# Optimization experiments

Hardware: AMD Instinct MI355X
Metric: run time of the kernel (lower is better)

## Reference

```python
import jax, jax.numpy as jnp
import numpy as np

HEADS = 8


def _attn_1d(xs, w_qkv, w_proj, heads, scale):
    """xs: [N, C, L] -> [N, C, L]. 1x1 conv == channel matmul."""
    n, c, l = xs.shape
    inner = w_proj.shape[1]
    d = inner // heads
    qkv = jnp.einsum('oc,ncl->nol', w_qkv, xs)          # [N, 3*inner, L]
    q, k, v = jnp.split(qkv, 3, axis=1)                  # each [N, inner, L]
    # [N, heads, L, d]
    q = q.reshape(n, heads, d, l).transpose(0, 1, 3, 2)
    k = k.reshape(n, heads, d, l).transpose(0, 1, 3, 2)
    v = v.reshape(n, heads, d, l).transpose(0, 1, 3, 2)
    attn = jax.nn.softmax(jnp.einsum('nhid,nhjd->nhij', q, k) * scale, axis=-1)
    out = jnp.einsum('nhij,nhjd->nhid', attn, v)         # [N, heads, L, d]
    out = out.transpose(0, 1, 3, 2).reshape(n, inner, l) # [N, inner, L]
    return jnp.einsum('co,nol->ncl', w_proj, out)


def _axial(x, w_qkv, w_proj, heads, scale, axis):
    b, c, h, w = x.shape
    if axis == 'h':
        xs = x.transpose(0, 3, 1, 2).reshape(b * w, c, h)
        out = _attn_1d(xs, w_qkv, w_proj, heads, scale)
        return out.reshape(b, w, c, h).transpose(0, 2, 3, 1)
    else:
        xs = x.transpose(0, 2, 1, 3).reshape(b * h, c, w)
        out = _attn_1d(xs, w_qkv, w_proj, heads, scale)
        return out.reshape(b, h, c, w).transpose(0, 2, 1, 3)


def setup_inputs() -> dict:
    key = jax.random.key(0)
    k1, k2, k3 = jax.random.split(key, 3)
    B, C, H, W = 4, 512, 128, 128
    heads = HEADS
    head_dim = C // heads
    inner = head_dim * heads
    x = jax.random.normal(k1, (B, C, H, W), dtype=jnp.float32)
    w_qkv = jax.random.normal(k2, (inner * 3, C), dtype=jnp.float32) * 0.02
    w_proj = jax.random.normal(k3, (C, inner), dtype=jnp.float32) * 0.02
    return {"x": x, "w_qkv": w_qkv, "w_proj": w_proj}


def reference(x, w_qkv, w_proj):
    c = x.shape[1]
    head_dim = c // HEADS
    scale = head_dim ** (-0.5)
    h_out = _axial(x, w_qkv, w_proj, HEADS, scale, 'h')
    w_out = _axial(h_out, w_qkv, w_proj, HEADS, scale, 'w')
    return x + w_out
```

## Files before the change

kernel.cpp:

```cpp
#include <hip/hip_runtime.h>
#include <hip/hip_bf16.h>
#include <stdint.h>

#define B_ 4
#define S_ 128
#define CH 512

typedef __attribute__((ext_vector_type(8))) __bf16 bf16x8;
typedef __attribute__((ext_vector_type(4))) float  f32x4;

__device__ __forceinline__ unsigned short f2b(float f) {
    union { float f; unsigned u; } v; v.f = f;
    unsigned r = v.u + 0x7FFFu + ((v.u >> 16) & 1u);
    return (unsigned short)(r >> 16);
}

#define GLD_LDS16(gp, lp) \
    __builtin_amdgcn_global_load_lds((const __attribute__((address_space(1))) void*)(gp), \
                                     (__attribute__((address_space(3))) void*)(lp), 16, 0, 0)

__global__ void cvt_w(const float* __restrict__ wq, const float* __restrict__ wp,
                      unsigned short* __restrict__ wqb, unsigned short* __restrict__ wpb) {
    int idx = (blockIdx.x * 256 + threadIdx.x) * 4;
    const float* s; unsigned short* d; int off;
    if (idx < 1536 * 512) { s = wq; d = wqb; off = idx; }
    else                  { s = wp; d = wpb; off = idx - 1536 * 512; }
    float4 v = *(const float4*)(s + off);
    ushort4 o; o.x = f2b(v.x); o.y = f2b(v.y); o.z = f2b(v.z); o.w = f2b(v.w);
    *(ushort4*)(d + off) = o;
}

__global__ __launch_bounds__(256) void k0_tr(const float* __restrict__ x,
                                             unsigned short* __restrict__ xb) {
    __shared__ unsigned short t[64][72];
    int bid = blockIdx.x;
    int ct = bid & 7, wt = (bid >> 3) & 1, h = (bid >> 4) & 127, b = bid >> 11;
    int tid = threadIdx.x;
    int c0 = ct * 64, w0 = wt * 64;
    const float* xp = x + ((size_t)b * CH * S_ + h) * S_;
    int wl = (tid & 15) * 4;
#pragma unroll
    for (int it = 0; it < 4; ++it) {
        int c = it * 16 + (tid >> 4);
        float4 v = *(const float4*)(xp + (size_t)(c0 + c) * (S_ * S_) + w0 + wl);
        t[wl + 0][c] = f2b(v.x);
        t[wl + 1][c] = f2b(v.y);
        t[wl + 2][c] = f2b(v.z);
        t[wl + 3][c] = f2b(v.w);
    }
    __syncthreads();
#pragma unroll
    for (int it = 0; it < 2; ++it) {
        int w = it * 32 + (tid >> 3);
        int ce = (tid & 7) * 8;
        int4 v = *(const int4*)&t[w][ce];
        size_t p = (size_t)((b * 128 + w0 + w) * 128 + h);
        *(int4*)(xb + p * 512 + c0 + ce) = v;
    }
}

template<int EPI>
__global__ __launch_bounds__(512, 2) void gemm8(
    const unsigned short* __restrict__ A,
    const unsigned short* __restrict__ Bm,
    unsigned short* __restrict__ outb,
    const float* __restrict__ xres,
    float* __restrict__ outf,
    int Mtiles)
{
    __shared__ unsigned short lds[65536];
    const int NT = 8;
    int nwg = gridDim.x;
    int wg = (blockIdx.x & 7) * (nwg >> 3) + (blockIdx.x >> 3);
    int mb = wg % Mtiles, nb = wg / Mtiles;
    int m0 = mb * 256, n0 = nb * 256;
    int tid = threadIdx.x, lane = tid & 63, wid = tid >> 6;
    int wm = wid >> 2, wn = wid & 3;

    f32x4 acc[8][4] = {};

    int l15  = lane & 15;
    int rsw  = ((lane >> 2) & 3) << 4;
    int cA0  = ((lane >> 4) * 8) ^ rsw;
    int cA1  = (32 + (lane >> 4) * 8) ^ rsw;
    int arow = (wm * 64 + l15) * 64;
    int brow = (wn * 32 + l15) * 64;

    int srow = tid >> 3;
    int scol = ((tid & 7) * 8) ^ (((srow >> 2) & 3) << 4);
    const unsigned short* Ab0 = A  + (size_t)(m0 + srow) * 512 + scol;
    const unsigned short* Bb0 = Bm + (size_t)(n0 + (srow >> 5) * 64 + (srow & 31)) * 512 + scol;

#define STAGE_A(kt, reg) do {                                                  \
        unsigned short* lb_ = &lds[((((kt) & 1) * 2 + (reg)) * 8192)];         \
        const unsigned short* g_ = Ab0 + (size_t)(reg) * (64 * 512) + (kt) * 64;\
        GLD_LDS16(g_,             lb_ + wid * 512);                            \
        GLD_LDS16(g_ + 128 * 512, lb_ + 4096 + wid * 512);                     \
    } while (0)
#define STAGE_B(kt, reg) do {                                                  \
        unsigned short* lb_ = &lds[32768 + ((((kt) & 1) * 2 + (reg)) * 8192)]; \
        const unsigned short* g_ = Bb0 + (size_t)(reg) * (32 * 512) + (kt) * 64;\
        GLD_LDS16(g_,             lb_ + wid * 512);                            \
        GLD_LDS16(g_ + 128 * 512, lb_ + 4096 + wid * 512);                     \
    } while (0)

    STAGE_A(0, 0); STAGE_A(0, 1); STAGE_B(0, 0); STAGE_B(0, 1);
    STAGE_A(1, 0); STAGE_B(1, 0);
    asm volatile("s_waitcnt vmcnt(4)" ::: "memory");
    __builtin_amdgcn_s_barrier();

    for (int j = 0; j < NT; ++j) {
        int db = j & 1;
        bf16x8 af[4][2];
#pragma unroll
        for (int q = 0; q < 4; ++q) {
            const int mq = q >> 1, nq = q & 1;
            int bbase = 32768 + (db * 2 + nq) * 8192 + brow;
            if (nq == 0) {
                int abase = (db * 2 + mq) * 8192 + arow;
#pragma unroll
                for (int fr = 0; fr < 4; ++fr) {
                    af[fr][0] = *(const bf16x8*)&lds[abase + fr * 1024 + cA0];
                    af[fr][1] = *(const bf16x8*)&lds[abase + fr * 1024 + cA1];
                }
            }
            bf16x8 bq[2][2];
#pragma unroll
            for (int fb = 0; fb < 2; ++fb) {
                bq[fb][0] = *(const bf16x8*)&lds[bbase + fb * 1024 + cA0];
                bq[fb][1] = *(const bf16x8*)&lds[bbase + fb * 1024 + cA1];
            }
            if (q == 0)      { if (j + 1 < NT) STAGE_A(j + 1, 1); }
            else if (q == 1) { if (j + 1 < NT) STAGE_B(j + 1, 1); }
            else if (q == 2) { if (j + 2 < NT) STAGE_A(j + 2, 0); }
            else {
                if (j + 2 < NT) STAGE_B(j + 2, 0);
                if (j < NT - 2) asm volatile("s_waitcnt vmcnt(4)" ::: "memory");
                else            asm volatile("s_waitcnt vmcnt(0)" ::: "memory");
            }
            __builtin_amdgcn_s_barrier();
            asm volatile("s_waitcnt lgkmcnt(0)" ::: "memory");
            __builtin_amdgcn_s_setprio(1);
#pragma unroll
            for (int h = 0; h < 2; ++h)
#pragma unroll
                for (int fr = 0; fr < 4; ++fr)
#pragma unroll
                    for (int fb = 0; fb < 2; ++fb)
                        acc[mq * 4 + fr][nq * 2 + fb] = __builtin_amdgcn_mfma_f32_16x16x32_bf16(
                            af[fr][h], bq[fb][h], acc[mq * 4 + fr][nq * 2 + fb], 0, 0, 0);
            __builtin_amdgcn_s_setprio(0);
            __builtin_amdgcn_s_barrier();
        }
    }
#undef STAGE_A
#undef STAGE_B

#pragma unroll
    for (int mi = 0; mi < 8; ++mi) {
        int row0 = m0 + wm * 128 + (mi >> 2) * 64 + (mi & 3) * 16 + ((lane >> 4) << 2);
#pragma unroll
        for (int ni = 0; ni < 4; ++ni) {
            int col = n0 + wn * 64 + (ni >> 1) * 32 + (ni & 1) * 16 + (lane & 15);
            int i = col & 127, sq = (col >> 7) & 127, bb = col >> 14;
            f32x4 a4 = acc[mi][ni];
            if (EPI == 0) {
                int g = row0 >> 6, d0 = row0 & 63;
                if (g < 16) {
                    size_t base = ((size_t)(g * 4 + bb) * 16384 + (size_t)sq * 128 + i) * 64 + d0;
                    ushort4 o;
                    o.x = f2b(a4[0]); o.y = f2b(a4[1]); o.z = f2b(a4[2]); o.w = f2b(a4[3]);
                    *(ushort4*)(outb + base) = o;
                } else {
                    size_t base = ((size_t)(g * 4 + bb) * 8192 + (size_t)sq * 64 + d0) * 128 + i;
                    outb[base]       = f2b(a4[0]);
                    outb[base + 128] = f2b(a4[1]);
                    outb[base + 256] = f2b(a4[2]);
                    outb[base + 384] = f2b(a4[3]);
                }
            } else if (EPI == 1) {
                size_t p2 = ((size_t)bb * 128 + i) * 128 + sq;
                ushort4 o;
                o.x = f2b(a4[0]); o.y = f2b(a4[1]); o.z = f2b(a4[2]); o.w = f2b(a4[3]);
                *(ushort4*)(outb + p2 * 512 + row0) = o;
            } else {
                size_t base = (((size_t)bb * 512 + row0) * 128 + sq) * 128 + i;
#pragma unroll
                for (int r = 0; r < 4; ++r) {
                    size_t a_ = base + (size_t)r * 16384;
                    outf[a_] = xres[a_] + a4[r];
                }
            }
        }
    }
}

__global__ __launch_bounds__(256) void attn_k(const unsigned short* __restrict__ qkv,
                                              unsigned short* __restrict__ o2) {
    __shared__ unsigned short Qs[128 * 80];
    __shared__ unsigned short Ks[128 * 80];
    __shared__ unsigned short Vt[64 * 144];
    int bid = blockIdx.x;
    int t = bid & 7, sq = (bid >> 3) & 127, b = bid >> 10;
    int tid = threadIdx.x, lane = tid & 63, wv = tid >> 6;
    const unsigned short* qg = qkv + ((size_t)(t * 4 + b) * 16384 + (size_t)sq * 128) * 64;
    const unsigned short* kg = qkv + ((size_t)((8 + t) * 4 + b) * 16384 + (size_t)sq * 128) * 64;
    const unsigned short* vg = qkv + ((size_t)((16 + t) * 4 + b) * 8192 + (size_t)sq * 64) * 128;
    {
        int r = tid >> 3, d0 = (tid & 7) * 8;
#pragma unroll
        for (int it = 0; it < 4; ++it) {
            *(int4*)(Qs + (it * 32 + r) * 80 + d0) = *(const int4*)(qg + (it * 32 + r) * 64 + d0);
            *(int4*)(Ks + (it * 32 + r) * 80 + d0) = *(const int4*)(kg + (it * 32 + r) * 64 + d0);
        }
        int r2 = tid >> 4, i0 = (tid & 15) * 8;
#pragma unroll
        for (int it = 0; it < 4; ++it)
            *(int4*)(Vt + (it * 16 + r2) * 144 + i0) = *(const int4*)(vg + (it * 16 + r2) * 128 + i0);
    }
    __syncthreads();

    f32x4 st[8][2] = {};
#pragma unroll
    for (int kk = 0; kk < 2; ++kk) {
        int ko = kk * 32 + (lane >> 4) * 8;
        bf16x8 bq[2];
#pragma unroll
        for (int nt = 0; nt < 2; ++nt)
            bq[nt] = *(const bf16x8*)(Qs + (wv * 32 + nt * 16 + (lane & 15)) * 80 + ko);
#pragma unroll
        for (int mt = 0; mt < 8; ++mt) {
            bf16x8 ak = *(const bf16x8*)(Ks + (mt * 16 + (lane & 15)) * 80 + ko);
#pragma unroll
            for (int nt = 0; nt < 2; ++nt)
                st[mt][nt] = __builtin_amdgcn_mfma_f32_16x16x32_bf16(ak, bq[nt], st[mt][nt], 0, 0, 0);
        }
    }

    const float sc = 0.125f * 1.44269504088896f;
    float mx[2], rinv[2];
    unsigned ppk[8][2][2];
#pragma unroll
    for (int nt = 0; nt < 2; ++nt) {
        float m = -3.0e38f;
#pragma unroll
        for (int mt = 0; mt < 8; ++mt)
#pragma unroll
            for (int r = 0; r < 4; ++r)
                m = fmaxf(m, st[mt][nt][r]);
        m = fmaxf(m, __shfl_xor(m, 16));
        m = fmaxf(m, __shfl_xor(m, 32));
        mx[nt] = m * sc;
    }
#pragma unroll
    for (int nt = 0; nt < 2; ++nt) {
        float s = 0.f;
#pragma unroll
        for (int mt = 0; mt < 8; ++mt) {
            float p0 = exp2f(st[mt][nt][0] * sc - mx[nt]);
            float p1 = exp2f(st[mt][nt][1] * sc - mx[nt]);
            float p2 = exp2f(st[mt][nt][2] * sc - mx[nt]);
            float p3 = exp2f(st[mt][nt][3] * sc - mx[nt]);
            s += (p0 + p1) + (p2 + p3);
            ppk[mt][nt][0] = (unsigned)f2b(p0) | ((unsigned)f2b(p1) << 16);
            ppk[mt][nt][1] = (unsigned)f2b(p2) | ((unsigned)f2b(p3) << 16);
        }
        s += __shfl_xor(s, 16);
        s += __shfl_xor(s, 32);
        rinv[nt] = 1.0f / s;
    }

    f32x4 ov[4][2] = {};
    int g = lane >> 4;
    int ls0 = (lane & 15) | ((g & 1) << 5);
    int ls1 = ls0 | 16;
    int hi = g >> 1;
#pragma unroll
    for (int kt = 0; kt < 4; ++kt) {
        bf16x8 bp[2];
#pragma unroll
        for (int nt = 0; nt < 2; ++nt) {
            unsigned a0 = (unsigned)__shfl((int)ppk[2 * kt    ][nt][0], ls0);
            unsigned b0 = (unsigned)__shfl((int)ppk[2 * kt + 1][nt][0], ls0);
            unsigned a1 = (unsigned)__shfl((int)ppk[2 * kt    ][nt][1], ls0);
            unsigned b1 = (unsigned)__shfl((int)ppk[2 * kt + 1][nt][1], ls0);
            unsigned a2 = (unsigned)__shfl((int)ppk[2 * kt    ][nt][0], ls1);
            unsigned b2 = (unsigned)__shfl((int)ppk[2 * kt + 1][nt][0], ls1);
            unsigned a3 = (unsigned)__shfl((int)ppk[2 * kt    ][nt][1], ls1);
            unsigned b3 = (unsigned)__shfl((int)ppk[2 * kt + 1][nt][1], ls1);
            union { unsigned u[4]; bf16x8 v; } pk;
            pk.u[0] = hi ? b0 : a0;
            pk.u[1] = hi ? b1 : a1;
            pk.u[2] = hi ? b2 : a2;
            pk.u[3] = hi ? b3 : a3;
            bp[nt] = pk.v;
        }
#pragma unroll
        for (int dt = 0; dt < 4; ++dt) {
            bf16x8 av = *(const bf16x8*)(Vt + (dt * 16 + (lane & 15)) * 144 + kt * 32 + (lane >> 4) * 8);
#pragma unroll
            for (int nt = 0; nt < 2; ++nt)
                ov[dt][nt] = __builtin_amdgcn_mfma_f32_16x16x32_bf16(av, bp[nt], ov[dt][nt], 0, 0, 0);
        }
    }

#pragma unroll
    for (int dt = 0; dt < 4; ++dt) {
        int d0 = dt * 16 + (lane >> 4) * 4;
#pragma unroll
        for (int nt = 0; nt < 2; ++nt) {
            int i = wv * 32 + nt * 16 + (lane & 15);
            size_t p = ((size_t)(b * 128 + sq)) * 128 + i;
            ushort4 o;
            o.x = f2b(ov[dt][nt][0] * rinv[nt]);
            o.y = f2b(ov[dt][nt][1] * rinv[nt]);
            o.z = f2b(ov[dt][nt][2] * rinv[nt]);
            o.w = f2b(ov[dt][nt][3] * rinv[nt]);
            *(ushort4*)(o2 + p * 512 + t * 64 + d0) = o;
        }
    }
}

extern "C" void kernel_launch(void* const* d_in, const int* in_sizes, int n_in,
                              void* d_out, int out_size, void* d_ws, size_t ws_size,
                              hipStream_t stream) {
    const float* x  = (const float*)d_in[0];
    const float* wq = (const float*)d_in[1];
    const float* wp = (const float*)d_in[2];
    float* out = (float*)d_out;
    char* ws = (char*)d_ws;
    unsigned short* wqb = (unsigned short*)(ws);
    unsigned short* wpb = (unsigned short*)(ws + ((size_t)2 << 20));
    unsigned short* xb  = (unsigned short*)(ws + ((size_t)4 << 20));
    unsigned short* o2  = (unsigned short*)(ws + ((size_t)68 << 20));
    unsigned short* qkv = (unsigned short*)(ws + ((size_t)132 << 20));

    cvt_w<<<1024, 256, 0, stream>>>(wq, wp, wqb, wpb);
    k0_tr<<<8192, 256, 0, stream>>>(x, xb);
    gemm8<0><<<6 * 256, 512, 0, stream>>>(wqb, xb, qkv, nullptr, nullptr, 6);
    attn_k<<<4096, 256, 0, stream>>>(qkv, o2);
    gemm8<1><<<2 * 256, 512, 0, stream>>>(wpb, o2, xb, nullptr, nullptr, 2);
    gemm8<0><<<6 * 256, 512, 0, stream>>>(wqb, xb, qkv, nullptr, nullptr, 6);
    attn_k<<<4096, 256, 0, stream>>>(qkv, o2);
    gemm8<2><<<2 * 256, 512, 0, stream>>>(wpb, o2, nullptr, x, out, 2);
}
```

Baseline: 584.6 us.

## Reorder GEMM main loop to load all fragments up front and reuse quadrants

Restructures the bf16 GEMM main loop so each k-tile loads the A0/B0 fragments first, then B1/A1, and runs the four MFMA quadrants as (a0,b0),(a0,b1),(a1,b0),(a1,b1). Global-to-LDS staging of the next tiles is spread between the quadrants, and the prefetch depth drops so only A(j+2,0) runs ahead. The aim is to reduce LDS fragment reloads and waits by keeping both A halves in registers, at the cost of higher register pressure and less global prefetch distance. The earlier lgkmcnt waits are removed, so correctness relies on the compiler inserting waits for LDS reads.

Result: slower. 639.2 us (+9.3%).

```diff
diff --git a/kernel.cpp b/kernel.cpp
--- a/kernel.cpp
+++ b/kernel.cpp
@@ -105,54 +105,73 @@
     } while (0)
 
     STAGE_A(0, 0); STAGE_A(0, 1); STAGE_B(0, 0); STAGE_B(0, 1);
-    STAGE_A(1, 0); STAGE_B(1, 0);
-    asm volatile("s_waitcnt vmcnt(4)" ::: "memory");
+    STAGE_A(1, 0);
+    asm volatile("s_waitcnt vmcnt(2)" ::: "memory");
     __builtin_amdgcn_s_barrier();
 
+#define MFMA_Q(ar, br, mo, no)                                                 \
+    __builtin_amdgcn_s_setprio(1);                                             \
+    _Pragma("unroll")                                                          \
+    for (int h = 0; h < 2; ++h)                                                \
+        _Pragma("unroll")                                                      \
+        for (int fr = 0; fr < 4; ++fr)                                         \
+            _Pragma("unroll")                                                  \
+            for (int fb = 0; fb < 2; ++fb)                                     \
+                acc[(mo) + fr][(no) + fb] = __builtin_amdgcn_mfma_f32_16x16x32_bf16( \
+                    ar[fr][h], br[fb][h], acc[(mo) + fr][(no) + fb], 0, 0, 0); \
+    __builtin_amdgcn_s_setprio(0);
+
     for (int j = 0; j < NT; ++j) {
-        int db = j & 1;
-        bf16x8 af[4][2];
-#pragma unroll
-        for (int q = 0; q < 4; ++q) {
-            const int mq = q >> 1, nq = q & 1;
-            int bbase = 32768 + (db * 2 + nq) * 8192 + brow;
-            if (nq == 0) {
-                int abase = (db * 2 + mq) * 8192 + arow;
-#pragma unroll
-                for (int fr = 0; fr < 4; ++fr) {
-                    af[fr][0] = *(const bf16x8*)&lds[abase + fr * 1024 + cA0];
-                    af[fr][1] = *(const bf16x8*)&lds[abase + fr * 1024 + cA1];
-                }
-            }
-            bf16x8 bq[2][2];
+        const int db = j & 1;
+        bf16x8 a0[4][2], a1[4][2], b0[2][2], b1[2][2];
+        {
+            int ab = (db * 2 + 0) * 8192 + arow;
+            int bb = 32768 + (db * 2 + 0) * 8192 + brow;
+#pragma unroll
+            for (int fr = 0; fr < 4; ++fr) {
+                a0[fr][0] = *(const bf16x8*)&lds[ab + fr * 1024 + cA0];
+                a0[fr][1] = *(const bf16x8*)&lds[ab + fr * 1024 + cA1];
+            }
 #pragma unroll
             for (int fb = 0; fb < 2; ++fb) {
-                bq[fb][0] = *(const bf16x8*)&lds[bbase + fb * 1024 + cA0];
-                bq[fb][1] = *(const bf16x8*)&lds[bbase + fb * 1024 + cA1];
-            }
-            if (q == 0)      { if (j + 1 < NT) STAGE_A(j + 1, 1); }
-            else if (q == 1) { if (j + 1 < NT) STAGE_B(j + 1, 1); }
-            else if (q == 2) { if (j + 2 < NT) STAGE_A(j + 2, 0); }
-            else {
-                if (j + 2 < NT) STAGE_B(j + 2, 0);
-                if (j < NT - 2) asm volatile("s_waitcnt vmcnt(4)" ::: "memory");
-                else            asm volatile("s_waitcnt vmcnt(0)" ::: "memory");
-            }
-            __builtin_amdgcn_s_barrier();
-            asm volatile("s_waitcnt lgkmcnt(0)" ::: "memory");
-            __builtin_amdgcn_s_setprio(1);
-#pragma unroll
-            for (int h = 0; h < 2; ++h)
-#pragma unroll
-                for (int fr = 0; fr < 4; ++fr)
-#pragma unroll
-                    for (int fb = 0; fb < 2; ++fb)
-                        acc[mq * 4 + fr][nq * 2 + fb] = __builtin_amdgcn_mfma_f32_16x16x32_bf16(
-                            af[fr][h], bq[fb][h], acc[mq * 4 + fr][nq * 2 + fb], 0, 0, 0);
-            __builtin_amdgcn_s_setprio(0);
-            __builtin_amdgcn_s_barrier();
-        }
-    }
+                b0[fb][0] = *(const bf16x8*)&lds[bb + fb * 1024 + cA0];
+                b0[fb][1] = *(const bf16x8*)&lds[bb + fb * 1024 + cA1];
+            }
+        }
+        if (j + 1 < NT) STAGE_A(j + 1, 1);
+        __builtin_amdgcn_s_barrier();
+        MFMA_Q(a0, b0, 0, 0)
+        __builtin_amdgcn_s_barrier();
+        {
+            int ab = (db * 2 + 1) * 8192 + arow;
+            int bb = 32768 + (db * 2 + 1) * 8192 + brow;
+#pragma unroll
+            for (int fb = 0; fb < 2; ++fb) {
+                b1[fb][0] = *(const bf16x8*)&lds[bb + fb * 1024 + cA0];
+                b1[fb][1] = *(const bf16x8*)&lds[bb + fb * 1024 + cA1];
+            }
+#pragma unroll
+            for (int fr = 0; fr < 4; ++fr) {
+                a1[fr][0] = *(const bf16x8*)&lds[ab + fr * 1024 + cA0];
+                a1[fr][1] = *(const bf16x8*)&lds[ab + fr * 1024 + cA1];
+            }
+        }
+        if (j + 1 < NT) STAGE_B(j + 1, 0);
+        __builtin_amdgcn_s_barrier();
+        MFMA_Q(a0, b1, 0, 2)
+        __builtin_amdgcn_s_barrier();
+        if (j + 1 < NT) STAGE_B(j + 1, 1);
+        __builtin_amdgcn_s_barrier();
+        MFMA_Q(a1, b0, 4, 0)
+        __builtin_amdgcn_s_barrier();
+        if (j + 2 < NT) STAGE_A(j + 2, 0);
+        if (j < NT - 2) asm volatile("s_waitcnt vmcnt(2)" ::: "memory");
+        else            asm volatile("s_waitcnt vmcnt(0)" ::: "memory");
+        __builtin_amdgcn_s_barrier();
+        MFMA_Q(a1, b1, 4, 2)
+        __builtin_amdgcn_s_barrier();
+    }
+#undef MFMA_Q
 #undef STAGE_A
 #undef STAGE_B
 
```
